# Kernel tuning notes

Hardware: AMD Instinct MI355X
Metric: run time of the kernel (lower is better)

The kernel has to match this reference:

```python
import jax, jax.numpy as jnp
import numpy as np

FP16_HUGE = 2.0 ** 15
NUM_HEAD = 4
LN_EPS = 1e-5


def setup_inputs() -> dict:
    key = jax.random.key(0)
    ks = jax.random.split(key, 12)
    B, N, D = 1, 256, 128
    H = NUM_HEAD
    inp = {
        "pair_act": jax.random.normal(ks[0], (B, N, N, D), dtype=jnp.float32),
        "pair_mask": jnp.ones((B, N, N), dtype=jnp.float32),
        "ln_scale": jnp.ones((D,), dtype=jnp.float32),
        "ln_bias": jnp.zeros((D,), dtype=jnp.float32),
        # torch Linear weight layout: [out_dim, in_dim]; applied as x @ W.T
        "w2d": jax.random.normal(ks[1], (H, D), dtype=jnp.float32) / np.sqrt(D),
        "wq": jax.random.normal(ks[2], (D, D), dtype=jnp.float32) / np.sqrt(D),
        "wk": jax.random.normal(ks[3], (D, D), dtype=jnp.float32) / np.sqrt(D),
        "wv": jax.random.normal(ks[4], (D, D), dtype=jnp.float32) / np.sqrt(D),
        "wg": jax.random.normal(ks[5], (D, D), dtype=jnp.float32) / np.sqrt(D),
        "bg": jnp.ones((D,), dtype=jnp.float32),  # gating bias init = 1.0
        "wo": jax.random.normal(ks[6], (D, D), dtype=jnp.float32) * 0.02,
        "bo": jnp.zeros((D,), dtype=jnp.float32),
    }
    return inp


def reference(pair_act, pair_mask, ln_scale, ln_bias, w2d, wq, wk, wv, wg, bg, wo, bo):
    B, N, _, D = pair_act.shape
    H = NUM_HEAD
    kd = D // H  # per-head key/value dim
    scale = kd ** (-0.5)

    # mask bias: [B, N(row), 1, 1, N(key)]
    bias = (FP16_HUGE * (pair_mask - 1.0))[:, :, None, None, :]

    # LayerNorm (fp32, eps=1e-5)
    mu = jnp.mean(pair_act, axis=-1, keepdims=True)
    var = jnp.mean(jnp.square(pair_act - mu), axis=-1, keepdims=True)
    x = (pair_act - mu) * jax.lax.rsqrt(var + LN_EPS) * ln_scale + ln_bias

    # non-batched per-head bias: [B, 1, H, N, N]
    nb = jnp.einsum("bijd,hd->bhij", x, w2d)[:, None]

    q = (x @ wq.T).reshape(B, N, N, H, kd) * scale  # [B, r, i, H, kd]
    k = (x @ wk.T).reshape(B, N, N, H, kd)
    v = (x @ wv.T).reshape(B, N, N, H, kd)

    logits = jnp.einsum("brihk,brjhk->brhij", q, k) + bias + nb  # [B, r, H, i, j]
    w = jax.nn.softmax(logits, axis=-1)
    o = jnp.einsum("brhij,brjhv->brihv", w, v)  # [B, r, i, H, kd]

    g = jax.nn.sigmoid(x @ wg.T + bg).reshape(B, N, N, H, kd)
    o = (o * g).reshape(B, N, N, D)

    out = o @ wo.T + bo
    return out * pair_mask[..., None]
```

## Files before the change

### kernel.cpp

```cpp
#include <hip/hip_runtime.h>
#include <hip/hip_bf16.h>

typedef unsigned short u16;
typedef __attribute__((ext_vector_type(8))) short bf16x8;
typedef __attribute__((ext_vector_type(4))) float f32x4;
typedef __attribute__((address_space(3))) unsigned lds_u32;
typedef const __attribute__((address_space(1))) unsigned glb_u32;

#define N 256
#define D 128
#define NH 4
#define KD 32
#define NN 65536
#define QK_SCALE 0.17677669529663687f
#define HUGE_MASK 32768.0f

__device__ __forceinline__ float b2f(u16 s) {
  union { float f; unsigned u; } x; x.u = ((unsigned)s) << 16; return x.f;
}
__device__ __forceinline__ u16 f2b(float f) {
  union { float f; unsigned u; } x; x.f = f;
  unsigned r = x.u + 0x7fff + ((x.u >> 16) & 1);
  return (u16)(r >> 16);
}

__global__ __launch_bounds__(256) void prep_w_kernel(
    const float* __restrict__ wq, const float* __restrict__ wk,
    const float* __restrict__ wv, const float* __restrict__ wg,
    const float* __restrict__ wo, u16* __restrict__ wb)
{
  int idx = blockIdx.x * 256 + threadIdx.x;
  const float* srcs[5] = {wq, wk, wv, wg, wo};
  int mat = idx >> 11, rem = idx & 2047;
  int row = rem >> 4, g = rem & 15;
  int gp = (g + (row & 15)) & 15;
  const float* s = srcs[mat] + row * 128 + g * 8;
  float4 f0 = *(const float4*)(s);
  float4 f1 = *(const float4*)(s + 4);
  uint4 pk;
  pk.x = (unsigned)f2b(f0.x) | ((unsigned)f2b(f0.y) << 16);
  pk.y = (unsigned)f2b(f0.z) | ((unsigned)f2b(f0.w) << 16);
  pk.z = (unsigned)f2b(f1.x) | ((unsigned)f2b(f1.y) << 16);
  pk.w = (unsigned)f2b(f1.z) | ((unsigned)f2b(f1.w) << 16);
  *(uint4*)(wb + (size_t)mat * 16384 + row * 128 + gp * 8) = pk;
}

__device__ __forceinline__ void async_stage(const u16* __restrict__ gsrc, u16* lds, int tid) {
  int lane = tid & 63, wave = tid >> 6;
  u16* lbase = lds + wave * 512;
  const u16* gbase = gsrc + wave * 512 + lane * 8;
#pragma unroll
  for (int p = 0; p < 8; p++) {
    __builtin_amdgcn_global_load_lds((glb_u32*)(gbase + p * 2048),
                                     (lds_u32*)(lbase + p * 2048), 16, 0, 0);
  }
}

__global__ __launch_bounds__(256) void projln_kernel(
    const float* __restrict__ pa, const float* __restrict__ lns, const float* __restrict__ lnb,
    const float* __restrict__ w2d, const u16* __restrict__ wb, const float* __restrict__ bg,
    u16* __restrict__ q, u16* __restrict__ k, u16* __restrict__ v, u16* __restrict__ g,
    float* __restrict__ nbT)
{
  __shared__ __align__(16) u16 Wl[2][16384];
  int tid = threadIdx.x;
  int wave = tid >> 6, lane = tid & 63;
  int lr = lane & 15, quad = lane >> 4;

  async_stage(wb, Wl[0], tid);

  bf16x8 a[2][4];
#pragma unroll
  for (int mt = 0; mt < 2; mt++) {
    int row = blockIdx.x * 128 + wave * 32 + mt * 16 + lr;
    const float* rp = pa + (size_t)row * D;
    float xv[4][8];
    float s = 0.f, ss = 0.f;
#pragma unroll
    for (int ks = 0; ks < 4; ks++) {
      float4 a0 = *(const float4*)(rp + ks * 32 + quad * 8);
      float4 a1 = *(const float4*)(rp + ks * 32 + quad * 8 + 4);
      xv[ks][0] = a0.x; xv[ks][1] = a0.y; xv[ks][2] = a0.z; xv[ks][3] = a0.w;
      xv[ks][4] = a1.x; xv[ks][5] = a1.y; xv[ks][6] = a1.z; xv[ks][7] = a1.w;
#pragma unroll
      for (int j = 0; j < 8; j++) { s += xv[ks][j]; ss += xv[ks][j] * xv[ks][j]; }
    }
    s  += __shfl_xor(s, 16, 64);  ss += __shfl_xor(ss, 16, 64);
    s  += __shfl_xor(s, 32, 64);  ss += __shfl_xor(ss, 32, 64);
    float mu = s * (1.0f / D);
    float var = ss * (1.0f / D) - mu * mu;
    float rs = rsqrtf(var + 1e-5f);
#pragma unroll
    for (int ks = 0; ks < 4; ks++) {
      float4 s0 = *(const float4*)(lns + ks * 32 + quad * 8);
      float4 s1 = *(const float4*)(lns + ks * 32 + quad * 8 + 4);
      float4 b0 = *(const float4*)(lnb + ks * 32 + quad * 8);
      float4 b1 = *(const float4*)(lnb + ks * 32 + quad * 8 + 4);
      float sc[8] = {s0.x,s0.y,s0.z,s0.w,s1.x,s1.y,s1.z,s1.w};
      float bi[8] = {b0.x,b0.y,b0.z,b0.w,b1.x,b1.y,b1.z,b1.w};
#pragma unroll
      for (int j = 0; j < 8; j++) xv[ks][j] = (xv[ks][j] - mu) * rs * sc[j] + bi[j];
    }
#pragma unroll
    for (int h = 0; h < NH; h++) {
      float p = 0.f;
#pragma unroll
      for (int ks = 0; ks < 4; ks++) {
        float4 w0 = *(const float4*)(w2d + h * D + ks * 32 + quad * 8);
        float4 w1 = *(const float4*)(w2d + h * D + ks * 32 + quad * 8 + 4);
        p += xv[ks][0]*w0.x + xv[ks][1]*w0.y + xv[ks][2]*w0.z + xv[ks][3]*w0.w
           + xv[ks][4]*w1.x + xv[ks][5]*w1.y + xv[ks][6]*w1.z + xv[ks][7]*w1.w;
      }
      p += __shfl_xor(p, 16, 64);
      p += __shfl_xor(p, 32, 64);
      if (quad == 0)
        nbT[(size_t)h * NN + (size_t)(row & 255) * 256 + (row >> 8)] = p;
    }
#pragma unroll
    for (int ks = 0; ks < 4; ks++)
#pragma unroll
      for (int j = 0; j < 8; j++) a[mt][ks][j] = (short)f2b(xv[ks][j]);
  }
  __syncthreads();

  u16* Os[4] = {q, k, v, g};
#pragma unroll
  for (int mat = 0; mat < 4; mat++) {
    if (mat < 3) async_stage(wb + (size_t)(mat + 1) * 16384, Wl[(mat + 1) & 1], tid);
    const u16* Wcur = Wl[mat & 1];
    f32x4 acc[2][2][4];
#pragma unroll
    for (int mt = 0; mt < 2; mt++)
#pragma unroll
      for (int tg = 0; tg < 2; tg++)
#pragma unroll
        for (int e = 0; e < 4; e++) acc[mt][tg][e] = (f32x4){0.f, 0.f, 0.f, 0.f};
#pragma unroll
    for (int ks = 0; ks < 4; ks++) {
#pragma unroll
      for (int tg = 0; tg < 2; tg++) {
#pragma unroll
        for (int e = 0; e < 4; e++) {
          int nrow = tg * 64 + 4 * lr + e;
          int gp = (ks * 4 + quad + (nrow & 15)) & 15;
          bf16x8 b = *(const bf16x8*)(&Wcur[nrow * 128 + gp * 8]);
          acc[0][tg][e] = __builtin_amdgcn_mfma_f32_16x16x32_bf16(a[0][ks], b, acc[0][tg][e], 0, 0, 0);
          acc[1][tg][e] = __builtin_amdgcn_mfma_f32_16x16x32_bf16(a[1][ks], b, acc[1][tg][e], 0, 0, 0);
        }
      }
    }
    u16* O = Os[mat];
#pragma unroll
    for (int mt = 0; mt < 2; mt++) {
      int row0 = blockIdx.x * 128 + wave * 32 + mt * 16 + quad * 4;
#pragma unroll
      for (int tg = 0; tg < 2; tg++) {
        int c0 = tg * 64 + 4 * lr;
        float bg0 = 0.f, bg1 = 0.f, bg2 = 0.f, bg3 = 0.f;
        if (mat == 3) { bg0 = bg[c0]; bg1 = bg[c0+1]; bg2 = bg[c0+2]; bg3 = bg[c0+3]; }
#pragma unroll
        for (int reg = 0; reg < 4; reg++) {
          float v0 = acc[mt][tg][0][reg], v1 = acc[mt][tg][1][reg];
          float v2 = acc[mt][tg][2][reg], v3 = acc[mt][tg][3][reg];
          if (mat == 0) { v0 *= QK_SCALE; v1 *= QK_SCALE; v2 *= QK_SCALE; v3 *= QK_SCALE; }
          if (mat == 3) {
            v0 = 1.0f / (1.0f + __expf(-(v0 + bg0)));
            v1 = 1.0f / (1.0f + __expf(-(v1 + bg1)));
            v2 = 1.0f / (1.0f + __expf(-(v2 + bg2)));
            v3 = 1.0f / (1.0f + __expf(-(v3 + bg3)));
          }
          uint2 pk;
          pk.x = (unsigned)f2b(v0) | ((unsigned)f2b(v1) << 16);
          pk.y = (unsigned)f2b(v2) | ((unsigned)f2b(v3) << 16);
          *(uint2*)(O + (size_t)(row0 + reg) * D + c0) = pk;
        }
      }
    }
    __syncthreads();
  }
}

__global__ __launch_bounds__(256) void attn_kernel(
    const u16* __restrict__ q, const u16* __restrict__ k, const u16* __restrict__ v,
    const u16* __restrict__ g, const float* __restrict__ nbT, const float* __restrict__ mask,
    u16* __restrict__ og)
{
  __shared__ __align__(16) u16 Kf[8192];
  __shared__ __align__(16) u16 Vf[8192];
  __shared__ __align__(16) u16 Pf[16384];
  __shared__ float bias_lds[256];
  int h = blockIdx.x & 3, r = blockIdx.x >> 2;
  int tid = threadIdx.x;
  {
    int j = tid;
    const u16* krow = k + ((size_t)r * N + j) * D + h * KD;
    int t = j >> 4, lrj = j & 15;
#pragma unroll
    for (int qc = 0; qc < 4; qc++)
      *(bf16x8*)(&Kf[((t * 4 + qc) * 16 + lrj) * 8]) = *(const bf16x8*)(krow + qc * 8);
    const u16* vrow = v + ((size_t)r * N + j) * D + h * KD;
    int ks = j >> 5, qj = (j >> 3) & 3, jj = j & 7;
#pragma unroll
    for (int c = 0; c < 32; c++)
      Vf[(((ks * 2 + (c & 1)) * 4 + qj) * 16 + (c >> 1)) * 8 + jj] = vrow[c];
    bias_lds[tid] = HUGE_MASK * (mask[r * N + tid] - 1.0f);
  }
  __syncthreads();
  int wave = tid >> 6, lane = tid & 63;
  int lr = lane & 15, quad = lane >> 4;
  u16* Pw = &Pf[wave * 4096];
  float bias_v[16];
#pragma unroll
  for (int t = 0; t < 16; t++) bias_v[t] = bias_lds[t * 16 + lr];
  const float* nbh = nbT + (size_t)h * NN;

  for (int pass = 0; pass < 4; pass++) {
    int i0 = pass * 64 + wave * 16;
    bf16x8 af = *(const bf16x8*)(q + ((size_t)r * N + i0 + lr) * D + h * KD + quad * 8);
    f32x4 S[16];
#pragma unroll
    for (int t = 0; t < 16; t++) {
      bf16x8 bfr = *(const bf16x8*)(&Kf[((t * 4 + quad) * 16 + lr) * 8]);
      S[t] = __builtin_amdgcn_mfma_f32_16x16x32_bf16(af, bfr, (f32x4){0.f,0.f,0.f,0.f}, 0, 0, 0);
    }
    float mx[4] = {-3e38f, -3e38f, -3e38f, -3e38f};
#pragma unroll
    for (int t = 0; t < 16; t++) {
      float4 nb4 = *(const float4*)(nbh + (size_t)(t * 16 + lr) * N + i0 + quad * 4);
      float bl = bias_v[t];
      S[t][0] += nb4.x + bl;  S[t][1] += nb4.y + bl;
      S[t][2] += nb4.z + bl;  S[t][3] += nb4.w + bl;
      mx[0] = fmaxf(mx[0], S[t][0]); mx[1] = fmaxf(mx[1], S[t][1]);
      mx[2] = fmaxf(mx[2], S[t][2]); mx[3] = fmaxf(mx[3], S[t][3]);
    }
#pragma unroll
    for (int reg = 0; reg < 4; reg++) {
#pragma unroll
      for (int off = 8; off; off >>= 1)
        mx[reg] = fmaxf(mx[reg], __shfl_xor(mx[reg], off, 16));
    }
    float lsum[4] = {0.f, 0.f, 0.f, 0.f};
#pragma unroll
    for (int t = 0; t < 16; t++) {
      int j = t * 16 + lr;
      int cbase = ((j >> 5) * 4 + ((j >> 3) & 3)) * 128 + (j & 7);
#pragma unroll
      for (int reg = 0; reg < 4; reg++) {
        float p = __expf(S[t][reg] - mx[reg]);
        lsum[reg] += p;
        union { float f; unsigned u; } cv; cv.f = p;
        Pw[cbase + (quad * 4 + reg) * 8] = (u16)((cv.u + 0x8000u) >> 16);
      }
    }
#pragma unroll
    for (int reg = 0; reg < 4; reg++) {
#pragma unroll
      for (int off = 8; off; off >>= 1)
        lsum[reg] += __shfl_xor(lsum[reg], off, 16);
    }
    __asm__ __volatile__("s_waitcnt lgkmcnt(0)" ::: "memory");
    f32x4 o[2] = {(f32x4){0.f,0.f,0.f,0.f}, (f32x4){0.f,0.f,0.f,0.f}};
#pragma unroll
    for (int ks = 0; ks < 8; ks++) {
      bf16x8 pa = *(const bf16x8*)(&Pw[((ks * 4 + quad) * 16 + lr) * 8]);
#pragma unroll
      for (int e = 0; e < 2; e++) {
        bf16x8 vb = *(const bf16x8*)(&Vf[(((ks * 2 + e) * 4 + quad) * 16 + lr) * 8]);
        o[e] = __builtin_amdgcn_mfma_f32_16x16x32_bf16(pa, vb, o[e], 0, 0, 0);
      }
    }
#pragma unroll
    for (int reg = 0; reg < 4; reg++) {
      float inv = __builtin_amdgcn_rcpf(lsum[reg]);
      int i = i0 + quad * 4 + reg;
      size_t base = ((size_t)r * N + i) * D + h * KD + 2 * lr;
      unsigned gv = *(const unsigned*)(g + base);
      float r0 = o[0][reg] * inv * b2f((u16)(gv & 0xffff));
      float r1 = o[1][reg] * inv * b2f((u16)(gv >> 16));
      *(unsigned*)(og + base) = (unsigned)f2b(r0) | ((unsigned)f2b(r1) << 16);
    }
  }
}

__global__ __launch_bounds__(256) void out_kernel(
    const u16* __restrict__ og, const u16* __restrict__ wob, const float* __restrict__ bo,
    const float* __restrict__ mask, float* __restrict__ out)
{
  __shared__ __align__(16) u16 Wlds[16384];
  int tid = threadIdx.x;
  async_stage(wob, Wlds, tid);
  int wave = tid >> 6, lane = tid & 63;
  int lr = lane & 15, quad = lane >> 4;
  bf16x8 a[2][4];
#pragma unroll
  for (int mt = 0; mt < 2; mt++) {
    int arow = blockIdx.x * 128 + wave * 32 + mt * 16 + lr;
#pragma unroll
    for (int ks = 0; ks < 4; ks++)
      a[mt][ks] = *(const bf16x8*)(og + (size_t)arow * D + ks * 32 + quad * 8);
  }
  __syncthreads();
  f32x4 acc[2][2][4];
#pragma unroll
  for (int mt = 0; mt < 2; mt++)
#pragma unroll
    for (int tg = 0; tg < 2; tg++)
#pragma unroll
      for (int e = 0; e < 4; e++) acc[mt][tg][e] = (f32x4){0.f, 0.f, 0.f, 0.f};
#pragma unroll
  for (int ks = 0; ks < 4; ks++) {
#pragma unroll
    for (int tg = 0; tg < 2; tg++) {
#pragma unroll
      for (int e = 0; e < 4; e++) {
        int nrow = tg * 64 + 4 * lr + e;
        int gp = (ks * 4 + quad + (nrow & 15)) & 15;
        bf16x8 b = *(const bf16x8*)(&Wlds[nrow * 128 + gp * 8]);
        acc[0][tg][e] = __builtin_amdgcn_mfma_f32_16x16x32_bf16(a[0][ks], b, acc[0][tg][e], 0, 0, 0);
        acc[1][tg][e] = __builtin_amdgcn_mfma_f32_16x16x32_bf16(a[1][ks], b, acc[1][tg][e], 0, 0, 0);
      }
    }
  }
#pragma unroll
  for (int mt = 0; mt < 2; mt++) {
    int row0 = blockIdx.x * 128 + wave * 32 + mt * 16 + quad * 4;
#pragma unroll
    for (int tg = 0; tg < 2; tg++) {
      int c0 = tg * 64 + 4 * lr;
      float4 bo4 = *(const float4*)(bo + c0);
#pragma unroll
      for (int reg = 0; reg < 4; reg++) {
        int pos = row0 + reg;
        float m = mask[pos];
        float4 o4;
        o4.x = (acc[mt][tg][0][reg] + bo4.x) * m;
        o4.y = (acc[mt][tg][1][reg] + bo4.y) * m;
        o4.z = (acc[mt][tg][2][reg] + bo4.z) * m;
        o4.w = (acc[mt][tg][3][reg] + bo4.w) * m;
        *(float4*)(out + (size_t)pos * D + c0) = o4;
      }
    }
  }
}

extern "C" void kernel_launch(void* const* d_in, const int* in_sizes, int n_in,
                              void* d_out, int out_size, void* d_ws, size_t ws_size,
                              hipStream_t stream)
{
  const float* pa   = (const float*)d_in[0];
  const float* mask = (const float*)d_in[1];
  const float* lns  = (const float*)d_in[2];
  const float* lnb  = (const float*)d_in[3];
  const float* w2d  = (const float*)d_in[4];
  const float* wq   = (const float*)d_in[5];
  const float* wk   = (const float*)d_in[6];
  const float* wv   = (const float*)d_in[7];
  const float* wg   = (const float*)d_in[8];
  const float* bg   = (const float*)d_in[9];
  const float* wo   = (const float*)d_in[10];
  const float* bo   = (const float*)d_in[11];

  const size_t ARR = (size_t)NN * D;
  u16* q  = (u16*)d_ws;
  u16* k  = q + ARR;
  u16* v  = k + ARR;
  u16* g  = v + ARR;
  u16* og = g + ARR;
  float* nbT = (float*)(og + ARR);
  u16* wb = (u16*)(nbT + (size_t)NH * NN);

  prep_w_kernel<<<40, 256, 0, stream>>>(wq, wk, wv, wg, wo, wb);
  projln_kernel<<<512, 256, 0, stream>>>(pa, lns, lnb, w2d, wb, bg, q, k, v, g, nbT);
  attn_kernel<<<N * NH, 256, 0, stream>>>(q, k, v, g, nbT, mask, og);
  out_kernel<<<512, 256, 0, stream>>>(og, wb + 4 * 16384, bo, mask, (float*)d_out);
}
```

Measured before the change: 187.0 us.

## Compute transposed S so softmax probabilities stay in registers, drop LDS P staging

```diff
diff --git a/kernel.cpp b/kernel.cpp
--- a/kernel.cpp
+++ b/kernel.cpp
@@ -60,7 +60,7 @@
     const float* __restrict__ pa, const float* __restrict__ lns, const float* __restrict__ lnb,
     const float* __restrict__ w2d, const u16* __restrict__ wb, const float* __restrict__ bg,
     u16* __restrict__ q, u16* __restrict__ k, u16* __restrict__ v, u16* __restrict__ g,
-    float* __restrict__ nbT)
+    float* __restrict__ nb)
 {
   __shared__ __align__(16) u16 Wl[2][16384];
   int tid = threadIdx.x;
@@ -114,7 +114,7 @@
       p += __shfl_xor(p, 16, 64);
       p += __shfl_xor(p, 32, 64);
       if (quad == 0)
-        nbT[(size_t)h * NN + (size_t)(row & 255) * 256 + (row >> 8)] = p;
+        nb[(size_t)h * NN + row] = p;
     }
 #pragma unroll
     for (int ks = 0; ks < 4; ks++)
@@ -180,14 +180,13 @@
   }
 }
 
-__global__ __launch_bounds__(256) void attn_kernel(
+__global__ __launch_bounds__(256, 4) void attn_kernel(
     const u16* __restrict__ q, const u16* __restrict__ k, const u16* __restrict__ v,
-    const u16* __restrict__ g, const float* __restrict__ nbT, const float* __restrict__ mask,
+    const u16* __restrict__ g, const float* __restrict__ nb, const float* __restrict__ mask,
     u16* __restrict__ og)
 {
   __shared__ __align__(16) u16 Kf[8192];
   __shared__ __align__(16) u16 Vf[8192];
-  __shared__ __align__(16) u16 Pf[16384];
   __shared__ float bias_lds[256];
   int h = blockIdx.x & 3, r = blockIdx.x >> 2;
   int tid = threadIdx.x;
@@ -199,79 +198,79 @@
     for (int qc = 0; qc < 4; qc++)
       *(bf16x8*)(&Kf[((t * 4 + qc) * 16 + lrj) * 8]) = *(const bf16x8*)(krow + qc * 8);
     const u16* vrow = v + ((size_t)r * N + j) * D + h * KD;
-    int ks = j >> 5, qj = (j >> 3) & 3, jj = j & 7;
+    int ksrc = j >> 5, jrel = j & 31;
+    int qv, jv;
+    if (jrel < 16) { qv = jrel >> 2; jv = jrel & 3; }
+    else           { qv = (jrel & 15) >> 2; jv = 4 + (jrel & 3); }
 #pragma unroll
     for (int c = 0; c < 32; c++)
-      Vf[(((ks * 2 + (c & 1)) * 4 + qj) * 16 + (c >> 1)) * 8 + jj] = vrow[c];
+      Vf[(((ksrc * 2 + (c & 1)) * 4 + qv) * 16 + (c >> 1)) * 8 + jv] = vrow[c];
     bias_lds[tid] = HUGE_MASK * (mask[r * N + tid] - 1.0f);
   }
   __syncthreads();
   int wave = tid >> 6, lane = tid & 63;
   int lr = lane & 15, quad = lane >> 4;
-  u16* Pw = &Pf[wave * 4096];
-  float bias_v[16];
-#pragma unroll
-  for (int t = 0; t < 16; t++) bias_v[t] = bias_lds[t * 16 + lr];
-  const float* nbh = nbT + (size_t)h * NN;
+  const float* nbh = nb + (size_t)h * NN;
 
   for (int pass = 0; pass < 4; pass++) {
     int i0 = pass * 64 + wave * 16;
-    bf16x8 af = *(const bf16x8*)(q + ((size_t)r * N + i0 + lr) * D + h * KD + quad * 8);
+    int irow = i0 + lr;
+    bf16x8 af = *(const bf16x8*)(q + ((size_t)r * N + irow) * D + h * KD + quad * 8);
     f32x4 S[16];
 #pragma unroll
     for (int t = 0; t < 16; t++) {
-      bf16x8 bfr = *(const bf16x8*)(&Kf[((t * 4 + quad) * 16 + lr) * 8]);
-      S[t] = __builtin_amdgcn_mfma_f32_16x16x32_bf16(af, bfr, (f32x4){0.f,0.f,0.f,0.f}, 0, 0, 0);
-    }
-    float mx[4] = {-3e38f, -3e38f, -3e38f, -3e38f};
+      bf16x8 kfr = *(const bf16x8*)(&Kf[((t * 4 + quad) * 16 + lr) * 8]);
+      S[t] = __builtin_amdgcn_mfma_f32_16x16x32_bf16(kfr, af, (f32x4){0.f,0.f,0.f,0.f}, 0, 0, 0);
+    }
+    float mx0 = -3e38f, mx1 = -3e38f, mx2 = -3e38f, mx3 = -3e38f;
+    const float* nbrow = nbh + (size_t)irow * N;
 #pragma unroll
     for (int t = 0; t < 16; t++) {
-      float4 nb4 = *(const float4*)(nbh + (size_t)(t * 16 + lr) * N + i0 + quad * 4);
-      float bl = bias_v[t];
-      S[t][0] += nb4.x + bl;  S[t][1] += nb4.y + bl;
-      S[t][2] += nb4.z + bl;  S[t][3] += nb4.w + bl;
-      mx[0] = fmaxf(mx[0], S[t][0]); mx[1] = fmaxf(mx[1], S[t][1]);
-      mx[2] = fmaxf(mx[2], S[t][2]); mx[3] = fmaxf(mx[3], S[t][3]);
-    }
-#pragma unroll
-    for (int reg = 0; reg < 4; reg++) {
-#pragma unroll
-      for (int off = 8; off; off >>= 1)
-        mx[reg] = fmaxf(mx[reg], __shfl_xor(mx[reg], off, 16));
-    }
-    float lsum[4] = {0.f, 0.f, 0.f, 0.f};
+      int jb = t * 16 + quad * 4;
+      float4 nb4 = *(const float4*)(nbrow + jb);
+      float4 b4  = *(const float4*)(&bias_lds[jb]);
+      S[t][0] += nb4.x + b4.x;  S[t][1] += nb4.y + b4.y;
+      S[t][2] += nb4.z + b4.z;  S[t][3] += nb4.w + b4.w;
+      mx0 = fmaxf(mx0, S[t][0]); mx1 = fmaxf(mx1, S[t][1]);
+      mx2 = fmaxf(mx2, S[t][2]); mx3 = fmaxf(mx3, S[t][3]);
+    }
+    float mx = fmaxf(fmaxf(mx0, mx1), fmaxf(mx2, mx3));
+    mx = fmaxf(mx, __shfl_xor(mx, 16, 64));
+    mx = fmaxf(mx, __shfl_xor(mx, 32, 64));
+    float ls0 = 0.f, ls1 = 0.f;
+    unsigned pw[32];
 #pragma unroll
     for (int t = 0; t < 16; t++) {
-      int j = t * 16 + lr;
-      int cbase = ((j >> 5) * 4 + ((j >> 3) & 3)) * 128 + (j & 7);
-#pragma unroll
-      for (int reg = 0; reg < 4; reg++) {
-        float p = __expf(S[t][reg] - mx[reg]);
-        lsum[reg] += p;
-        union { float f; unsigned u; } cv; cv.f = p;
-        Pw[cbase + (quad * 4 + reg) * 8] = (u16)((cv.u + 0x8000u) >> 16);
-      }
-    }
-#pragma unroll
-    for (int reg = 0; reg < 4; reg++) {
-#pragma unroll
-      for (int off = 8; off; off >>= 1)
-        lsum[reg] += __shfl_xor(lsum[reg], off, 16);
-    }
-    __asm__ __volatile__("s_waitcnt lgkmcnt(0)" ::: "memory");
+      float p0 = __expf(S[t][0] - mx);
+      float p1 = __expf(S[t][1] - mx);
+      float p2 = __expf(S[t][2] - mx);
+      float p3 = __expf(S[t][3] - mx);
+      ls0 += p0 + p1;  ls1 += p2 + p3;
+      union { float f; unsigned u; } u0, u1, u2, u3;
+      u0.f = p0; u1.f = p1; u2.f = p2; u3.f = p3;
+      pw[t * 2]     = ((u0.u + 0x8000u) >> 16) | ((u1.u + 0x8000u) & 0xffff0000u);
+      pw[t * 2 + 1] = ((u2.u + 0x8000u) >> 16) | ((u3.u + 0x8000u) & 0xffff0000u);
+    }
+    float lsum = ls0 + ls1;
+    lsum += __shfl_xor(lsum, 16, 64);
+    lsum += __shfl_xor(lsum, 32, 64);
+    float invd = __builtin_amdgcn_rcpf(lsum);
+
     f32x4 o[2] = {(f32x4){0.f,0.f,0.f,0.f}, (f32x4){0.f,0.f,0.f,0.f}};
 #pragma unroll
     for (int ks = 0; ks < 8; ks++) {
-      bf16x8 pa = *(const bf16x8*)(&Pw[((ks * 4 + quad) * 16 + lr) * 8]);
+      union { bf16x8 v; unsigned u[4]; } pa;
+      pa.u[0] = pw[ks * 4];     pa.u[1] = pw[ks * 4 + 1];
+      pa.u[2] = pw[ks * 4 + 2]; pa.u[3] = pw[ks * 4 + 3];
 #pragma unroll
       for (int e = 0; e < 2; e++) {
         bf16x8 vb = *(const bf16x8*)(&Vf[(((ks * 2 + e) * 4 + quad) * 16 + lr) * 8]);
-        o[e] = __builtin_amdgcn_mfma_f32_16x16x32_bf16(pa, vb, o[e], 0, 0, 0);
+        o[e] = __builtin_amdgcn_mfma_f32_16x16x32_bf16(pa.v, vb, o[e], 0, 0, 0);
       }
     }
 #pragma unroll
     for (int reg = 0; reg < 4; reg++) {
-      float inv = __builtin_amdgcn_rcpf(lsum[reg]);
+      float inv = __shfl(invd, quad * 4 + reg, 64);
       int i = i0 + quad * 4 + reg;
       size_t base = ((size_t)r * N + i) * D + h * KD + 2 * lr;
       unsigned gv = *(const unsigned*)(g + base);
@@ -366,11 +365,11 @@
   u16* v  = k + ARR;
   u16* g  = v + ARR;
   u16* og = g + ARR;
-  float* nbT = (float*)(og + ARR);
-  u16* wb = (u16*)(nbT + (size_t)NH * NN);
+  float* nb = (float*)(og + ARR);
+  u16* wb = (u16*)(nb + (size_t)NH * NN);
 
   prep_w_kernel<<<40, 256, 0, stream>>>(wq, wk, wv, wg, wo, wb);
-  projln_kernel<<<512, 256, 0, stream>>>(pa, lns, lnb, w2d, wb, bg, q, k, v, g, nbT);
-  attn_kernel<<<N * NH, 256, 0, stream>>>(q, k, v, g, nbT, mask, og);
+  projln_kernel<<<512, 256, 0, stream>>>(pa, lns, lnb, w2d, wb, bg, q, k, v, g, nb);
+  attn_kernel<<<N * NH, 256, 0, stream>>>(q, k, v, g, nb, mask, og);
   out_kernel<<<512, 256, 0, stream>>>(og, wb + 4 * 16384, bo, mask, (float*)d_out);
 }
```

Result: slower. 323.5 us (+73.0%).
